# Kernel optimization log

Measured on AMD Instinct MI355X. Metric: run time of the kernel, lower is better.

## Reference

```python
import jax, jax.numpy as jnp
import numpy as np

ALPHA = 0.34          # Ewald splitting parameter (init kwarg alpha)
MAX_HKL = 12          # init kwarg max_hkl
TWO_PI = 2.0 * np.pi


def setup_inputs() -> dict:
    key = jax.random.key(0)
    k1, k2 = jax.random.split(key)
    N = 4096
    L = 40.0  # cubic box edge (Angstrom)
    coords = jax.random.uniform(k1, (N, 3), dtype=jnp.float32) * L
    q = jax.random.normal(k2, (N,), dtype=jnp.float32)
    q = q - jnp.mean(q)  # neutral cell (k=0 term is excluded)
    box = jnp.eye(3, dtype=jnp.float32) * L
    return {"coords": coords, "box": box, "q": q}


def _ewald_recip_energy(coords, box, q):
    """Reciprocal-space Ewald sum over |h|,|k|,|l| <= MAX_HKL (rank=0 PME fallback).

    pot_i = (4*pi/V) * sum_{k!=0} exp(-|k|^2/(4 a^2))/|k|^2 * Re[S(k) exp(-i k.r_i)]
    E     = 0.5 * sum_i q_i * pot_i
    """
    K = MAX_HKL
    vol = jnp.abs(jnp.linalg.det(box))
    recip = TWO_PI * jnp.linalg.inv(box).T  # rows = reciprocal lattice vectors (3,3)
    h = jnp.arange(-K, K + 1)
    hh, kk, ll = jnp.meshgrid(h, h, h, indexing="ij")
    hkl = jnp.stack([hh.ravel(), kk.ravel(), ll.ravel()], axis=-1).astype(jnp.float32)  # (Nk,3)
    kvecs = hkl @ recip                      # (Nk,3)
    k2 = jnp.sum(kvecs * kvecs, axis=-1)     # (Nk,)
    nonzero = k2 > 0.0                       # mask out k = 0 (static shape, jit-safe)
    k2_safe = jnp.where(nonzero, k2, 1.0)
    inv_4a2 = 1.0 / (4.0 * ALPHA * ALPHA)
    fac = jnp.where(nonzero, jnp.exp(-k2_safe * inv_4a2) / k2_safe, 0.0)  # (Nk,)
    phases = coords @ kvecs.T                # (N, Nk)
    c = jnp.cos(phases)
    s = jnp.sin(phases)
    Sre = q @ c                              # (Nk,) Re S(k)
    Sim = q @ s                              # (Nk,) Im S(k)
    pref = (4.0 * np.pi) / vol
    # Re[S(k) e^{-i k.r_i}] = Sre*cos + Sim*sin
    pot = pref * (c @ (fac * Sre) + s @ (fac * Sim))  # (N,)
    return 0.5 * jnp.sum(q * pot)


def reference(coords, box, q):
    return _ewald_recip_energy(coords, box, q)
```

## Files before the change

### kernel.cpp

```cpp
#include <hip/hip_runtime.h>
#include <math.h>

namespace {
constexpr int   KMAX  = 12;
constexpr int   NLINE = 313;
constexpr int   NL25  = 25;
constexpr int   NKV   = NLINE * NL25;
constexpr int   KDIM  = 4096;
constexpr int   NKS   = 32;
constexpr int   KC    = KDIM / NKS;
constexpr int   MROWS = 640;
constexpr int   NCOLS = 64;
constexpr int   S2_BLOCKS = (NKV + 255) / 256;
constexpr float ALPHA_  = 0.34f;
constexpr float TWO_PI_ = 6.283185307179586f;

typedef __attribute__((ext_vector_type(4))) _Float16 half4;
typedef __attribute__((ext_vector_type(8))) _Float16 half8;
typedef __attribute__((ext_vector_type(4))) float    f32x4;
}

__device__ __forceinline__ void cofactors(const float* __restrict__ box,
                                          float C[3][3], float* det) {
  const float b00 = box[0], b01 = box[1], b02 = box[2];
  const float b10 = box[3], b11 = box[4], b12 = box[5];
  const float b20 = box[6], b21 = box[7], b22 = box[8];
  C[0][0] =  (b11 * b22 - b12 * b21);
  C[0][1] = -(b10 * b22 - b12 * b20);
  C[0][2] =  (b10 * b21 - b11 * b20);
  C[1][0] = -(b01 * b22 - b02 * b21);
  C[1][1] =  (b00 * b22 - b02 * b20);
  C[1][2] = -(b00 * b21 - b01 * b20);
  C[2][0] =  (b01 * b12 - b02 * b11);
  C[2][1] = -(b00 * b12 - b02 * b10);
  C[2][2] =  (b00 * b11 - b01 * b10);
  *det = b00 * C[0][0] + b01 * C[0][1] + b02 * C[0][2];
}

__device__ __forceinline__ void line_hk(int L, int* h, int* k) {
  if (L < 300)      { *h = L / 25 + 1; *k = L % 25 - 12; }
  else if (L < 312) { *h = 0;          *k = L - 299;     }
  else              { *h = 0;          *k = 0;           }
}

__global__ __launch_bounds__(256) void build_gemm(
    const float* __restrict__ coords, const float* __restrict__ box,
    const float* __restrict__ q, int N,
    float* __restrict__ Cp, float* __restrict__ out)
{
  __shared__ _Float16 Al[4][32][16][4];
  __shared__ _Float16 Bl[4][32][16][4];

  const int mtg = blockIdx.x;
  const int ks  = blockIdx.y;
  if (mtg == 0 && ks == 0 && threadIdx.x == 0) out[0] = 0.0f;

  float C[3][3], det;
  cofactors(box, C, &det);
  const float invdet = 1.0f / det;

  for (int it = 0; it < 32; ++it) {
    const int e    = threadIdx.x + it * 256;
    const int k0   = e & 3;
    const int rp   = (e >> 2) & 7;
    const int kt   = (e >> 5) & 31;
    const int tile = (e >> 10) & 3;
    const bool isA = e < 4096;
    const int  i   = ks * KC + kt * 4 + k0;
    float v0 = 0.f, v1 = 0.f;
    if (i < N) {
      const float x = coords[3 * i + 0];
      const float y = coords[3 * i + 1];
      const float z = coords[3 * i + 2];
      if (isA) {
        const int L = mtg * 32 + tile * 8 + rp;
        int h, k; line_hk(L, &h, &k);
        const float a = (x * C[0][0] + y * C[0][1] + z * C[0][2]) * invdet;
        const float b = (x * C[1][0] + y * C[1][1] + z * C[1][2]) * invdet;
        float t = fmaf((float)h, a, (float)k * b);
        float tf; asm("v_fract_f32 %0, %1" : "=v"(tf) : "v"(t));
        float s0, c0;
        asm("v_sin_f32 %0, %1" : "=v"(s0) : "v"(tf));
        asm("v_cos_f32 %0, %1" : "=v"(c0) : "v"(tf));
        const float qq = q[i];
        v0 = qq * c0; v1 = qq * s0;
      } else {
        const int ls = tile * 8 + rp;
        const int l  = ls - KMAX;
        const float c = (x * C[2][0] + y * C[2][1] + z * C[2][2]) * invdet;
        float t = (float)l * c;
        float tf; asm("v_fract_f32 %0, %1" : "=v"(tf) : "v"(t));
        float s0, c0;
        asm("v_sin_f32 %0, %1" : "=v"(s0) : "v"(tf));
        asm("v_cos_f32 %0, %1" : "=v"(c0) : "v"(tf));
        v0 = c0; v1 = s0;
      }
    }
    if (isA) {
      Al[tile][kt][2 * rp + 0][k0] = (_Float16)v0;
      Al[tile][kt][2 * rp + 1][k0] = (_Float16)v1;
    } else {
      Bl[tile][kt][2 * rp + 0][k0] = (_Float16)v0;
      Bl[tile][kt][2 * rp + 1][k0] = (_Float16)v1;
    }
  }
  __syncthreads();

  const int w    = threadIdx.x >> 6;
  const int lane = threadIdx.x & 63;
  const int r = lane & 15, g = lane >> 4;

  f32x4 acc0 = {0.f,0.f,0.f,0.f}, acc1 = {0.f,0.f,0.f,0.f};
  f32x4 acc2 = {0.f,0.f,0.f,0.f}, acc3 = {0.f,0.f,0.f,0.f};
#pragma unroll
  for (int s = 0; s < 4; ++s) {
    union { half4 h4[2]; half8 h8; } ua;
    ua.h4[0] = *(const half4*)&Al[w][s * 8 + g][r][0];
    ua.h4[1] = *(const half4*)&Al[w][s * 8 + 4 + g][r][0];
    union { half4 h4[2]; half8 h8; } ub;
    ub.h4[0] = *(const half4*)&Bl[0][s * 8 + g][r][0];
    ub.h4[1] = *(const half4*)&Bl[0][s * 8 + 4 + g][r][0];
    acc0 = __builtin_amdgcn_mfma_f32_16x16x32_f16(ua.h8, ub.h8, acc0, 0, 0, 0);
    ub.h4[0] = *(const half4*)&Bl[1][s * 8 + g][r][0];
    ub.h4[1] = *(const half4*)&Bl[1][s * 8 + 4 + g][r][0];
    acc1 = __builtin_amdgcn_mfma_f32_16x16x32_f16(ua.h8, ub.h8, acc1, 0, 0, 0);
    ub.h4[0] = *(const half4*)&Bl[2][s * 8 + g][r][0];
    ub.h4[1] = *(const half4*)&Bl[2][s * 8 + 4 + g][r][0];
    acc2 = __builtin_amdgcn_mfma_f32_16x16x32_f16(ua.h8, ub.h8, acc2, 0, 0, 0);
    ub.h4[0] = *(const half4*)&Bl[3][s * 8 + g][r][0];
    ub.h4[1] = *(const half4*)&Bl[3][s * 8 + 4 + g][r][0];
    acc3 = __builtin_amdgcn_mfma_f32_16x16x32_f16(ua.h8, ub.h8, acc3, 0, 0, 0);
  }

  float* base = Cp + ((size_t)ks * MROWS + mtg * 64 + w * 16) * NCOLS;
#pragma unroll
  for (int j = 0; j < 4; ++j) {
    base[(size_t)(g * 4 + j) * NCOLS +  0 + r] = acc0[j];
    base[(size_t)(g * 4 + j) * NCOLS + 16 + r] = acc1[j];
    base[(size_t)(g * 4 + j) * NCOLS + 32 + r] = acc2[j];
    base[(size_t)(g * 4 + j) * NCOLS + 48 + r] = acc3[j];
  }
}

__global__ __launch_bounds__(256) void stage2(
    const float* __restrict__ Cp, const float* __restrict__ box,
    float* __restrict__ out)
{
  __shared__ float red[256];
  const int idx = blockIdx.x * 256 + threadIdx.x;
  float e = 0.f;
  if (idx < NKV) {
    const int L  = idx / NL25;
    const int ls = idx % NL25;
    const int l  = ls - KMAX;
    int h, k; line_hk(L, &h, &k);
    if (!(h == 0 && k == 0 && l <= 0)) {
      float Sre = 0.f, Sim = 0.f;
      for (int s = 0; s < NKS; ++s) {
        const float* c0 = Cp + ((size_t)s * MROWS + 2 * L) * NCOLS;
        const float prr = c0[2 * ls + 0];
        const float pri = c0[2 * ls + 1];
        const float pir = c0[NCOLS + 2 * ls + 0];
        const float pii = c0[NCOLS + 2 * ls + 1];
        Sre += prr - pii;
        Sim += pri + pir;
      }
      float C[3][3], det;
      cofactors(box, C, &det);
      const float invdet = 1.0f / det;
      const float hf = (float)h, kf = (float)k, lf = (float)l;
      const float kx = (hf * C[0][0] + kf * C[1][0] + lf * C[2][0]) * invdet;
      const float ky = (hf * C[0][1] + kf * C[1][1] + lf * C[2][1]) * invdet;
      const float kz = (hf * C[0][2] + kf * C[1][2] + lf * C[2][2]) * invdet;
      const float k2 = TWO_PI_ * TWO_PI_ * (kx * kx + ky * ky + kz * kz);
      const float fac = __expf(-k2 / (4.0f * ALPHA_ * ALPHA_)) / k2;
      e = fac * fmaf(Sre, Sre, Sim * Sim);
    }
  }
  red[threadIdx.x] = e;
  __syncthreads();
  for (int s = 128; s > 0; s >>= 1) {
    if (threadIdx.x < s) red[threadIdx.x] += red[threadIdx.x + s];
    __syncthreads();
  }
  if (threadIdx.x == 0) {
    float C[3][3], det;
    cofactors(box, C, &det);
    const float scale = (4.0f * 3.14159265358979323846f) / fabsf(det);
    atomicAdd(out, scale * red[0]);
  }
}

extern "C" void kernel_launch(void* const* d_in, const int* in_sizes, int n_in,
                              void* d_out, int out_size, void* d_ws, size_t ws_size,
                              hipStream_t stream) {
  const float* coords = (const float*)d_in[0];
  const float* box    = (const float*)d_in[1];
  const float* q      = (const float*)d_in[2];
  float* out = (float*)d_out;
  const int N = in_sizes[2];

  float* Cp = (float*)d_ws;

  hipLaunchKernelGGL(build_gemm, dim3(10, NKS), dim3(256), 0, stream,
                     coords, box, q, N, Cp, out);
  hipLaunchKernelGGL(stage2, dim3(S2_BLOCKS), dim3(256), 0, stream,
                     Cp, box, out);
}
```

Before: 22.15 us.

## Double K-splits, transpose partial-sum layout, split stage2 reduction across four lanes

The GEMM kernel now uses 64 K-slices of 64 atoms instead of 32 of 128, doubling the grid to 640 blocks and halving per-block trig and LDS work. Partial results are stored with the split index innermost, so stage2 can read each k-vector's partials as contiguous float4 vectors. Stage2 gives each k-vector four threads that combine their sums with shuffles, replacing a strided 32-iteration loop. This costs more partial-sum memory and scattered strided writes in the first kernel.

```diff
diff --git a/kernel.cpp b/kernel.cpp
--- a/kernel.cpp
+++ b/kernel.cpp
@@ -6,12 +6,12 @@
 constexpr int   NLINE = 313;
 constexpr int   NL25  = 25;
 constexpr int   NKV   = NLINE * NL25;
-constexpr int   KDIM  = 4096;
-constexpr int   NKS   = 32;
-constexpr int   KC    = KDIM / NKS;
+constexpr int   NKS   = 64;
+constexpr int   KC    = 64;
 constexpr int   MROWS = 640;
 constexpr int   NCOLS = 64;
-constexpr int   S2_BLOCKS = (NKV + 255) / 256;
+constexpr int   S2_THREADS = NKV * 4;
+constexpr int   S2_BLOCKS  = (S2_THREADS + 255) / 256;
 constexpr float ALPHA_  = 0.34f;
 constexpr float TWO_PI_ = 6.283185307179586f;
 
@@ -48,8 +48,8 @@
     const float* __restrict__ q, int N,
     float* __restrict__ Cp, float* __restrict__ out)
 {
-  __shared__ _Float16 Al[4][32][16][4];
-  __shared__ _Float16 Bl[4][32][16][4];
+  __shared__ _Float16 Al[4][16][16][4];
+  __shared__ _Float16 Bl[4][16][16][4];
 
   const int mtg = blockIdx.x;
   const int ks  = blockIdx.y;
@@ -59,13 +59,14 @@
   cofactors(box, C, &det);
   const float invdet = 1.0f / det;
 
-  for (int it = 0; it < 32; ++it) {
+#pragma unroll
+  for (int it = 0; it < 16; ++it) {
     const int e    = threadIdx.x + it * 256;
     const int k0   = e & 3;
     const int rp   = (e >> 2) & 7;
-    const int kt   = (e >> 5) & 31;
-    const int tile = (e >> 10) & 3;
-    const bool isA = e < 4096;
+    const int kt   = (e >> 5) & 15;
+    const int tile = (e >> 9) & 3;
+    const bool isA = e < 2048;
     const int  i   = ks * KC + kt * 4 + k0;
     float v0 = 0.f, v1 = 0.f;
     if (i < N) {
@@ -113,7 +114,7 @@
   f32x4 acc0 = {0.f,0.f,0.f,0.f}, acc1 = {0.f,0.f,0.f,0.f};
   f32x4 acc2 = {0.f,0.f,0.f,0.f}, acc3 = {0.f,0.f,0.f,0.f};
 #pragma unroll
-  for (int s = 0; s < 4; ++s) {
+  for (int s = 0; s < 2; ++s) {
     union { half4 h4[2]; half8 h8; } ua;
     ua.h4[0] = *(const half4*)&Al[w][s * 8 + g][r][0];
     ua.h4[1] = *(const half4*)&Al[w][s * 8 + 4 + g][r][0];
@@ -132,13 +133,14 @@
     acc3 = __builtin_amdgcn_mfma_f32_16x16x32_f16(ua.h8, ub.h8, acc3, 0, 0, 0);
   }
 
-  float* base = Cp + ((size_t)ks * MROWS + mtg * 64 + w * 16) * NCOLS;
 #pragma unroll
   for (int j = 0; j < 4; ++j) {
-    base[(size_t)(g * 4 + j) * NCOLS +  0 + r] = acc0[j];
-    base[(size_t)(g * 4 + j) * NCOLS + 16 + r] = acc1[j];
-    base[(size_t)(g * 4 + j) * NCOLS + 32 + r] = acc2[j];
-    base[(size_t)(g * 4 + j) * NCOLS + 48 + r] = acc3[j];
+    const size_t R = (size_t)mtg * 64 + w * 16 + g * 4 + j;
+    float* rowp = Cp + (R * NCOLS) * NKS + ks;
+    rowp[(size_t)( 0 + r) * NKS] = acc0[j];
+    rowp[(size_t)(16 + r) * NKS] = acc1[j];
+    rowp[(size_t)(32 + r) * NKS] = acc2[j];
+    rowp[(size_t)(48 + r) * NKS] = acc3[j];
   }
 }
 
@@ -147,35 +149,49 @@
     float* __restrict__ out)
 {
   __shared__ float red[256];
-  const int idx = blockIdx.x * 256 + threadIdx.x;
+  const int tid = blockIdx.x * 256 + threadIdx.x;
+  const int kv  = tid >> 2;
+  const int sq  = tid & 3;
+  float Sre = 0.f, Sim = 0.f;
+  bool valid = false;
+  int h = 0, k = 0, l = 0;
+  if (kv < NKV) {
+    const int L  = kv / NL25;
+    const int ls = kv % NL25;
+    l = ls - KMAX;
+    line_hk(L, &h, &k);
+    valid = !(h == 0 && k == 0 && l <= 0);
+    if (valid) {
+      const float* prr = Cp + ((size_t)(2 * L + 0) * NCOLS + 2 * ls + 0) * NKS + sq * 16;
+      const float* pri = Cp + ((size_t)(2 * L + 0) * NCOLS + 2 * ls + 1) * NKS + sq * 16;
+      const float* pir = Cp + ((size_t)(2 * L + 1) * NCOLS + 2 * ls + 0) * NKS + sq * 16;
+      const float* pii = Cp + ((size_t)(2 * L + 1) * NCOLS + 2 * ls + 1) * NKS + sq * 16;
+#pragma unroll
+      for (int v = 0; v < 4; ++v) {
+        const float4 a = ((const float4*)prr)[v];
+        const float4 b = ((const float4*)pri)[v];
+        const float4 c = ((const float4*)pir)[v];
+        const float4 d = ((const float4*)pii)[v];
+        Sre += (a.x - d.x) + (a.y - d.y) + (a.z - d.z) + (a.w - d.w);
+        Sim += (b.x + c.x) + (b.y + c.y) + (b.z + c.z) + (b.w + c.w);
+      }
+    }
+  }
+  Sre += __shfl_xor(Sre, 1); Sre += __shfl_xor(Sre, 2);
+  Sim += __shfl_xor(Sim, 1); Sim += __shfl_xor(Sim, 2);
+
   float e = 0.f;
-  if (idx < NKV) {
-    const int L  = idx / NL25;
-    const int ls = idx % NL25;
-    const int l  = ls - KMAX;
-    int h, k; line_hk(L, &h, &k);
-    if (!(h == 0 && k == 0 && l <= 0)) {
-      float Sre = 0.f, Sim = 0.f;
-      for (int s = 0; s < NKS; ++s) {
-        const float* c0 = Cp + ((size_t)s * MROWS + 2 * L) * NCOLS;
-        const float prr = c0[2 * ls + 0];
-        const float pri = c0[2 * ls + 1];
-        const float pir = c0[NCOLS + 2 * ls + 0];
-        const float pii = c0[NCOLS + 2 * ls + 1];
-        Sre += prr - pii;
-        Sim += pri + pir;
-      }
-      float C[3][3], det;
-      cofactors(box, C, &det);
-      const float invdet = 1.0f / det;
-      const float hf = (float)h, kf = (float)k, lf = (float)l;
-      const float kx = (hf * C[0][0] + kf * C[1][0] + lf * C[2][0]) * invdet;
-      const float ky = (hf * C[0][1] + kf * C[1][1] + lf * C[2][1]) * invdet;
-      const float kz = (hf * C[0][2] + kf * C[1][2] + lf * C[2][2]) * invdet;
-      const float k2 = TWO_PI_ * TWO_PI_ * (kx * kx + ky * ky + kz * kz);
-      const float fac = __expf(-k2 / (4.0f * ALPHA_ * ALPHA_)) / k2;
-      e = fac * fmaf(Sre, Sre, Sim * Sim);
-    }
+  if (kv < NKV && valid && sq == 0) {
+    float C[3][3], det;
+    cofactors(box, C, &det);
+    const float invdet = 1.0f / det;
+    const float hf = (float)h, kf = (float)k, lf = (float)l;
+    const float kx = (hf * C[0][0] + kf * C[1][0] + lf * C[2][0]) * invdet;
+    const float ky = (hf * C[0][1] + kf * C[1][1] + lf * C[2][1]) * invdet;
+    const float kz = (hf * C[0][2] + kf * C[1][2] + lf * C[2][2]) * invdet;
+    const float k2 = TWO_PI_ * TWO_PI_ * (kx * kx + ky * ky + kz * kz);
+    const float fac = __expf(-k2 / (4.0f * ALPHA_ * ALPHA_)) / k2;
+    e = fac * fmaf(Sre, Sre, Sim * Sim);
   }
   red[threadIdx.x] = e;
   __syncthreads();
```

Result: slower. 33.00 us (+49.0%).
